# Kernel tuning notes

Hardware: AMD Instinct MI355X
Metric: run time of the kernel (lower is better)

## Reference

```python
import jax, jax.numpy as jnp
import numpy as np

NEG_BIG = -9e15  # matches -9000000000000000.0 in the torch source
ALPHA = 0.2      # LeakyReLU negative slope


def setup_inputs() -> dict:
    key = jax.random.key(0)
    k1, k2, k3, k4 = jax.random.split(key, 4)
    N, F_in, F_out = 8192, 256, 128
    x = jax.random.normal(k1, (N, F_in), dtype=jnp.float32)
    adj = jax.random.randint(k2, (N, N), 0, 2, dtype=jnp.int32)
    W = jax.random.normal(k3, (F_in, F_out), dtype=jnp.float32) * 0.05
    a = jax.random.normal(k4, (2 * F_out, 1), dtype=jnp.float32) * 0.05
    return {"x": x, "adj": adj, "W": W, "a": a}


def reference(x, adj, W, a):
    # h = x @ W : [N, F]
    h = x @ W
    F_out = W.shape[1]
    # Algebraically identical to the concat formulation:
    # a^T [h_i || h_j] = h_i @ a1 + h_j @ a2
    a1 = a[:F_out, 0]
    a2 = a[F_out:, 0]
    src = h @ a1  # [N]
    dst = h @ a2  # [N]
    e = jax.nn.leaky_relu(src[:, None] + dst[None, :], negative_slope=ALPHA)  # [N, N]
    attention = jnp.where(adj > 0, e, NEG_BIG)
    attention = jax.nn.softmax(attention, axis=1)
    # dropout is identity in eval mode (training=False)
    h_prime = attention @ h  # [N, F]
    return h_prime
```

## Files before the change

### kernel.cpp

```cpp
#include <hip/hip_runtime.h>
#include <cstdint>

#define N 8192
#define FIN 256
#define FOUT 128
#define ALPHA 0.2f
#define JP 4
#define JSL (N / JP)
#define TJ 64
#define NTILE (JSL / TJ)
#define RB 32

typedef unsigned short u16;
typedef __attribute__((ext_vector_type(8))) short short8;
typedef __attribute__((ext_vector_type(4))) float floatx4;

__device__ __forceinline__ u16 bf16_rne(float f) {
  uint32_t u = __float_as_uint(f);
  u += 0x7fff + ((u >> 16) & 1);
  return (u16)(u >> 16);
}

__device__ __forceinline__ void gl_lds16(const void* g, void* l) {
  __builtin_amdgcn_global_load_lds(
      (const __attribute__((address_space(1))) void*)g,
      (__attribute__((address_space(3))) void*)l, 16, 0, 0);
}

__global__ __launch_bounds__(256) void k_proj(const float* __restrict__ x,
                                              const float* __restrict__ W,
                                              const float* __restrict__ a,
                                              u16* __restrict__ hT3,
                                              float* __restrict__ srcv,
                                              float* __restrict__ dstv) {
  __shared__ float xs[8 * FIN];
  __shared__ float partS[4][4], partD[4][4];
  const int t = threadIdx.x;
  const int R0 = blockIdx.x * 8;

  const float4* xv = (const float4*)(x + (size_t)R0 * FIN);
  float4* xsv = (float4*)xs;
  xsv[t] = xv[t];
  xsv[t + 256] = xv[t + 256];
  __syncthreads();

  const int c  = t & 127;
  const int rg = (t >> 7) * 4;

  float acc[4] = {0.f, 0.f, 0.f, 0.f};
  float wa[4], wb[4];
  #pragma unroll
  for (int j = 0; j < 4; ++j) wa[j] = W[j * FOUT + c];
  #pragma unroll
  for (int j = 0; j < 4; ++j) wb[j] = W[(4 + j) * FOUT + c];

  for (int k4 = 0; k4 < FIN / 4; ++k4) {
    float wc[4];
    #pragma unroll
    for (int j = 0; j < 4; ++j) { wc[j] = wa[j]; wa[j] = wb[j]; }
    const int kn = (k4 + 2 < FIN / 4) ? k4 + 2 : k4;
    #pragma unroll
    for (int j = 0; j < 4; ++j) wb[j] = W[(kn * 4 + j) * FOUT + c];
    #pragma unroll
    for (int i = 0; i < 4; ++i) {
      const float4 xq = *(const float4*)&xs[(rg + i) * FIN + k4 * 4];
      acc[i] += xq.x * wc[0] + xq.y * wc[1] + xq.z * wc[2] + xq.w * wc[3];
    }
  }

  {
    const int j = R0 + rg;
    const int jb = j >> 5, q = (j >> 3) & 3, jj = j & 7;
    const int m = c & 15, nt = c >> 4;
    union { u16 u[4]; uint2 v; } pk;
    #pragma unroll
    for (int i = 0; i < 4; ++i) pk.u[i] = bf16_rne(acc[i]);
    *(uint2*)(hT3 + (size_t)(((jb * 8 + nt) * 64) + (m * 4 + q)) * 8 + jj) = pk.v;
  }

  const float a1 = a[c], a2 = a[FOUT + c];
  float s4[4], d4[4];
  #pragma unroll
  for (int i = 0; i < 4; ++i) { s4[i] = acc[i] * a1; d4[i] = acc[i] * a2; }
  #pragma unroll
  for (int off = 32; off > 0; off >>= 1) {
    #pragma unroll
    for (int i = 0; i < 4; ++i) {
      s4[i] += __shfl_down(s4[i], off);
      d4[i] += __shfl_down(d4[i], off);
    }
  }
  const int wv = t >> 6, lane = t & 63;
  if (lane == 0) {
    #pragma unroll
    for (int i = 0; i < 4; ++i) { partS[wv][i] = s4[i]; partD[wv][i] = d4[i]; }
  }
  __syncthreads();
  if (t < 16) {
    const int i = t & 3, rg2 = (t >> 2) & 1, which = t >> 3;
    if (which == 0) srcv[R0 + rg2 * 4 + i] = partS[rg2*2][i] + partS[rg2*2+1][i];
    else            dstv[R0 + rg2 * 4 + i] = partD[rg2*2][i] + partD[rg2*2+1][i];
  }
}

__global__ __launch_bounds__(256, 4) void k_gat(const int* __restrict__ adj,
                                                const u16* __restrict__ hT3,
                                                const float* __restrict__ srcv,
                                                const float* __restrict__ dstv,
                                                float* __restrict__ P,
                                                float* __restrict__ lp) {
  __shared__ u16 hS[2][8192];
  const int t = threadIdx.x;
  const int wv = t >> 6, lane = t & 63;
  const int q = lane >> 4, m = lane & 15;
  const int rg = wv & 1;
  const int cg = wv >> 1;
  const int bm = blockIdx.x & 255;
  const int jp = blockIdx.x >> 8;
  const int R0 = bm * RB;
  const int j0 = jp * JSL;
  const int Lq = m * 4 + q;

  const float srcm = srcv[R0 + rg * 16 + m];
  const int*   adjp = adj + (size_t)(R0 + rg * 16 + m) * N + j0 + q * 8;
  const float* dstp = dstv + j0 + q * 8;
  const size_t jb00 = (size_t)(j0 >> 5);

  floatx4 acc[4];
  #pragma unroll
  for (int nt = 0; nt < 4; ++nt) acc[nt] = (floatx4){0.f, 0.f, 0.f, 0.f};
  float lsum = 0.f;

  #define STAGE(I, BUF)                                                        \
  {                                                                            \
    _Pragma("unroll")                                                          \
    for (int cc = 0; cc < 4; ++cc) {                                           \
      const int kc = wv * 4 + cc;                                              \
      const int jbl = kc >> 3, nt_ = kc & 7;                                   \
      const u16* srcp = hT3 + ((jb00 + (size_t)(I) * 2 + jbl) * 8 + nt_) * 512 \
                        + (size_t)lane * 8;                                    \
      gl_lds16(srcp, &hS[BUF][kc * 512]);                                      \
    }                                                                          \
  }

  #define TILE_BODY(I, BUFR, BUFW,                                             \
                    CA0, CA1, CA2, CA3, CD0, CD1, CD2, CD3,                    \
                    NA0, NA1, NA2, NA3, ND0, ND1, ND2, ND3)                    \
  {                                                                            \
    __syncthreads();        \
    const int nx = ((I) + 1 < NTILE) ? (I) + 1 : (I);                          \
    NA0 = *(const int4*)(adjp + nx * TJ);                                      \
    NA1 = *(const int4*)(adjp + nx * TJ + 4);                                  \
    NA2 = *(const int4*)(adjp + nx * TJ + 32);                                 \
    NA3 = *(const int4*)(adjp + nx * TJ + 36);                                 \
    ND0 = *(const float4*)(dstp + nx * TJ);                                    \
    ND1 = *(const float4*)(dstp + nx * TJ + 4);                                \
    ND2 = *(const float4*)(dstp + nx * TJ + 32);                               \
    ND3 = *(const float4*)(dstp + nx * TJ + 36);                               \
    STAGE(nx, BUFW)                                                            \
    _Pragma("unroll")                                                          \
    for (int ks = 0; ks < 2; ++ks) {                                           \
      const int4   A0 = ks ? CA2 : CA0, A1 = ks ? CA3 : CA1;                   \
      const float4 D0 = ks ? CD2 : CD0, D1 = ks ? CD3 : CD1;                   \
      const int   ai[8] = {A0.x, A0.y, A0.z, A0.w, A1.x, A1.y, A1.z, A1.w};    \
      const float df[8] = {D0.x, D0.y, D0.z, D0.w, D1.x, D1.y, D1.z, D1.w};    \
      union { u16 u[8]; short8 s; } pk;                                        \
      _Pragma("unroll")                                                        \
      for (int e = 0; e < 8; ++e) {                                            \
        float v = srcm + df[e];                                                \
        v = fmaxf(v, ALPHA * v);                                               \
        const float p = ai[e] > 0 ? __expf(v) : 0.f;                           \
        lsum += p;                                                             \
        pk.u[e] = bf16_rne(p);                                                 \
      }                                                                        \
      _Pragma("unroll")                                                        \
      for (int nt = 0; nt < 4; ++nt) {                                         \
        const short8 bf =                                                      \
            *(const short8*)&hS[BUFR][(ks * 8 + cg * 4 + nt) * 512 + Lq * 8];  \
        acc[nt] =                                                              \
            __builtin_amdgcn_mfma_f32_16x16x32_bf16(pk.s, bf, acc[nt], 0, 0, 0); \
      }                                                                        \
    }                                                                          \
  }

  int4   aA0 = *(const int4*)(adjp),      aA1 = *(const int4*)(adjp + 4);
  int4   aA2 = *(const int4*)(adjp + 32), aA3 = *(const int4*)(adjp + 36);
  float4 dA0 = *(const float4*)(dstp),      dA1 = *(const float4*)(dstp + 4);
  float4 dA2 = *(const float4*)(dstp + 32), dA3 = *(const float4*)(dstp + 36);
  STAGE(0, 0)
  int4   aB0, aB1, aB2, aB3;
  float4 dB0, dB1, dB2, dB3;

  for (int i = 0; i < NTILE; i += 2) {
    TILE_BODY(i,     (i >> 1) & 0 ? 1 : 0, 1,
              aA0, aA1, aA2, aA3, dA0, dA1, dA2, dA3,
              aB0, aB1, aB2, aB3, dB0, dB1, dB2, dB3)
    TILE_BODY(i + 1, 1, 0,
              aB0, aB1, aB2, aB3, dB0, dB1, dB2, dB3,
              aA0, aA1, aA2, aA3, dA0, dA1, dA2, dA3)
  }
  #undef TILE_BODY
  #undef STAGE

  lsum += __shfl_xor(lsum, 16);
  lsum += __shfl_xor(lsum, 32);
  if (cg == 0 && lane < 16)
    lp[(size_t)jp * N + R0 + rg * 16 + lane] = lsum;

  float* Pp = P + ((size_t)jp * N + R0 + rg * 16) * FOUT + cg * 64;
  #pragma unroll
  for (int nt = 0; nt < 4; ++nt)
    #pragma unroll
    for (int ri = 0; ri < 4; ++ri)
      Pp[(size_t)(q * 4 + ri) * FOUT + nt * 16 + m] = acc[nt][ri];
}

__global__ __launch_bounds__(256) void k_norm(const float* __restrict__ P,
                                              const float* __restrict__ lp,
                                              float* __restrict__ out) {
  const int idx = blockIdx.x * 256 + threadIdx.x;
  const int rr = idx >> 5;
  const int c4 = (idx & 31) * 4;
  float l = 0.f;
  #pragma unroll
  for (int j = 0; j < JP; ++j) l += lp[j * N + rr];
  const float inv = 1.0f / l;
  float4 s = {0.f, 0.f, 0.f, 0.f};
  #pragma unroll
  for (int j = 0; j < JP; ++j) {
    const float4 p = *(const float4*)(P + ((size_t)j * N + rr) * FOUT + c4);
    s.x += p.x; s.y += p.y; s.z += p.z; s.w += p.w;
  }
  s.x *= inv; s.y *= inv; s.z *= inv; s.w *= inv;
  *(float4*)(out + (size_t)rr * FOUT + c4) = s;
}

extern "C" void kernel_launch(void* const* d_in, const int* in_sizes, int n_in,
                              void* d_out, int out_size, void* d_ws, size_t ws_size,
                              hipStream_t stream) {
  const float* x   = (const float*)d_in[0];
  const int*   adj = (const int*)d_in[1];
  const float* W   = (const float*)d_in[2];
  const float* a   = (const float*)d_in[3];
  float* out = (float*)d_out;

  char* ws = (char*)d_ws;
  u16*   hT3  = (u16*)ws;     ws += (size_t)FOUT * N * sizeof(u16);
  float* srcv = (float*)ws;   ws += (size_t)N * sizeof(float);
  float* dstv = (float*)ws;   ws += (size_t)N * sizeof(float);
  float* P    = (float*)ws;   ws += (size_t)JP * N * FOUT * sizeof(float);
  float* lp   = (float*)ws;   ws += (size_t)JP * N * sizeof(float);

  k_proj<<<N / 8, 256, 0, stream>>>(x, W, a, hT3, srcv, dstv);
  k_gat <<<256 * JP, 256, 0, stream>>>(adj, hT3, srcv, dstv, P, lp);
  k_norm<<<(N * FOUT / 4) / 256, 256, 0, stream>>>(P, lp, out);
}
```

Baseline: 456.7 us.

## Pack adjacency into bitmask in a separate pass before attention kernel

Adds a k_mask kernel that reads the int32 adjacency matrix once and packs it into a per-row bitmask using wave ballots. The attention kernel then reads 32x less mask data per tile instead of the full int32 adj rows. The adj/dst register double-buffering is replaced by a simpler loop that loads dst and mask words inline. The adj matrix still has to be read once in full, and in exchange the change adds a kernel launch and a mask buffer in workspace.

```diff
diff --git a/kernel.cpp b/kernel.cpp
--- a/kernel.cpp
+++ b/kernel.cpp
@@ -9,9 +9,9 @@
 #define JSL (N / JP)
 #define TJ 64
 #define NTILE (JSL / TJ)
-#define RB 32
 
 typedef unsigned short u16;
+typedef unsigned int u32;
 typedef __attribute__((ext_vector_type(8))) short short8;
 typedef __attribute__((ext_vector_type(4))) float floatx4;
 
@@ -103,26 +103,50 @@
   }
 }
 
-__global__ __launch_bounds__(256, 4) void k_gat(const int* __restrict__ adj,
+__global__ __launch_bounds__(256, 4) void k_mask(const int* __restrict__ adj,
+                                                 u32* __restrict__ mask) {
+  const int t = threadIdx.x, wv = t >> 6, lane = t & 63;
+  const int row = blockIdx.x * 4 + wv;
+  const int* ar = adj + (size_t)row * N;
+  u32* mr = mask + (size_t)row * (N / 32);
+  const int lh = lane >> 1, ll = lane & 1;
+
+  #pragma unroll 1
+  for (int c = 0; c < 4; ++c) {
+    int v[32];
+    #pragma unroll
+    for (int k = 0; k < 32; ++k) v[k] = ar[c * 2048 + k * 64 + lane];
+    u32 w = 0;
+    #pragma unroll
+    for (int k = 0; k < 32; ++k) {
+      const unsigned long long b = __ballot(v[k] > 0);
+      const u32 cand = ll ? (u32)(b >> 32) : (u32)b;
+      w = (lh == k) ? cand : w;
+    }
+    mr[c * 64 + lane] = w;
+  }
+}
+
+__global__ __launch_bounds__(256, 4) void k_gat(const u32* __restrict__ mask,
                                                 const u16* __restrict__ hT3,
                                                 const float* __restrict__ srcv,
                                                 const float* __restrict__ dstv,
                                                 float* __restrict__ P,
                                                 float* __restrict__ lp) {
   __shared__ u16 hS[2][8192];
-  const int t = threadIdx.x;
-  const int wv = t >> 6, lane = t & 63;
+  const int t = threadIdx.x, wv = t >> 6, lane = t & 63;
   const int q = lane >> 4, m = lane & 15;
   const int rg = wv & 1;
   const int cg = wv >> 1;
   const int bm = blockIdx.x & 255;
   const int jp = blockIdx.x >> 8;
-  const int R0 = bm * RB;
+  const int R0 = bm * 32;
   const int j0 = jp * JSL;
   const int Lq = m * 4 + q;
-
-  const float srcm = srcv[R0 + rg * 16 + m];
-  const int*   adjp = adj + (size_t)(R0 + rg * 16 + m) * N + j0 + q * 8;
+  const int row = R0 + rg * 16 + m;
+
+  const float srcm = srcv[row];
+  const u32*   mrow = mask + (size_t)row * (N / 32) + (j0 >> 5);
   const float* dstp = dstv + j0 + q * 8;
   const size_t jb00 = (size_t)(j0 >> 5);
 
@@ -143,64 +167,48 @@
     }                                                                          \
   }
 
-  #define TILE_BODY(I, BUFR, BUFW,                                             \
-                    CA0, CA1, CA2, CA3, CD0, CD1, CD2, CD3,                    \
-                    NA0, NA1, NA2, NA3, ND0, ND1, ND2, ND3)                    \
+  #define TILE_WORK(I, BUF)                                                    \
   {                                                                            \
-    __syncthreads();        \
-    const int nx = ((I) + 1 < NTILE) ? (I) + 1 : (I);                          \
-    NA0 = *(const int4*)(adjp + nx * TJ);                                      \
-    NA1 = *(const int4*)(adjp + nx * TJ + 4);                                  \
-    NA2 = *(const int4*)(adjp + nx * TJ + 32);                                 \
-    NA3 = *(const int4*)(adjp + nx * TJ + 36);                                 \
-    ND0 = *(const float4*)(dstp + nx * TJ);                                    \
-    ND1 = *(const float4*)(dstp + nx * TJ + 4);                                \
-    ND2 = *(const float4*)(dstp + nx * TJ + 32);                               \
-    ND3 = *(const float4*)(dstp + nx * TJ + 36);                               \
-    STAGE(nx, BUFW)                                                            \
+    const uint2  mw = *(const uint2*)(mrow + (I) * 2);                         \
+    const float4 D0 = *(const float4*)(dstp + (I) * 64);                       \
+    const float4 D1 = *(const float4*)(dstp + (I) * 64 + 4);                   \
+    const float4 D2 = *(const float4*)(dstp + (I) * 64 + 32);                  \
+    const float4 D3 = *(const float4*)(dstp + (I) * 64 + 36);                  \
     _Pragma("unroll")                                                          \
     for (int ks = 0; ks < 2; ++ks) {                                           \
-      const int4   A0 = ks ? CA2 : CA0, A1 = ks ? CA3 : CA1;                   \
-      const float4 D0 = ks ? CD2 : CD0, D1 = ks ? CD3 : CD1;                   \
-      const int   ai[8] = {A0.x, A0.y, A0.z, A0.w, A1.x, A1.y, A1.z, A1.w};    \
-      const float df[8] = {D0.x, D0.y, D0.z, D0.w, D1.x, D1.y, D1.z, D1.w};    \
+      const u32 byte8 = ((ks ? mw.y : mw.x) >> (q * 8)) & 0xffu;               \
+      const float4 Da = ks ? D2 : D0, Db = ks ? D3 : D1;                       \
+      const float df[8] = {Da.x, Da.y, Da.z, Da.w, Db.x, Db.y, Db.z, Db.w};    \
       union { u16 u[8]; short8 s; } pk;                                        \
       _Pragma("unroll")                                                        \
       for (int e = 0; e < 8; ++e) {                                            \
         float v = srcm + df[e];                                                \
         v = fmaxf(v, ALPHA * v);                                               \
-        const float p = ai[e] > 0 ? __expf(v) : 0.f;                           \
+        const float p = ((byte8 >> e) & 1u) ? __expf(v) : 0.f;                 \
         lsum += p;                                                             \
         pk.u[e] = bf16_rne(p);                                                 \
       }                                                                        \
       _Pragma("unroll")                                                        \
       for (int nt = 0; nt < 4; ++nt) {                                         \
         const short8 bf =                                                      \
-            *(const short8*)&hS[BUFR][(ks * 8 + cg * 4 + nt) * 512 + Lq * 8];  \
+            *(const short8*)&hS[BUF][(ks * 8 + cg * 4 + nt) * 512 + Lq * 8];   \
         acc[nt] =                                                              \
             __builtin_amdgcn_mfma_f32_16x16x32_bf16(pk.s, bf, acc[nt], 0, 0, 0); \
       }                                                                        \
     }                                                                          \
   }
 
-  int4   aA0 = *(const int4*)(adjp),      aA1 = *(const int4*)(adjp + 4);
-  int4   aA2 = *(const int4*)(adjp + 32), aA3 = *(const int4*)(adjp + 36);
-  float4 dA0 = *(const float4*)(dstp),      dA1 = *(const float4*)(dstp + 4);
-  float4 dA2 = *(const float4*)(dstp + 32), dA3 = *(const float4*)(dstp + 36);
   STAGE(0, 0)
-  int4   aB0, aB1, aB2, aB3;
-  float4 dB0, dB1, dB2, dB3;
-
   for (int i = 0; i < NTILE; i += 2) {
-    TILE_BODY(i,     (i >> 1) & 0 ? 1 : 0, 1,
-              aA0, aA1, aA2, aA3, dA0, dA1, dA2, dA3,
-              aB0, aB1, aB2, aB3, dB0, dB1, dB2, dB3)
-    TILE_BODY(i + 1, 1, 0,
-              aB0, aB1, aB2, aB3, dB0, dB1, dB2, dB3,
-              aA0, aA1, aA2, aA3, dA0, dA1, dA2, dA3)
-  }
-  #undef TILE_BODY
+    __syncthreads();
+    if (i + 1 < NTILE) STAGE(i + 1, 1)
+    TILE_WORK(i, 0)
+    __syncthreads();
+    if (i + 2 < NTILE) STAGE(i + 2, 0)
+    TILE_WORK(i + 1, 1)
+  }
   #undef STAGE
+  #undef TILE_WORK
 
   lsum += __shfl_xor(lsum, 16);
   lsum += __shfl_xor(lsum, 32);
@@ -223,7 +231,7 @@
   const int c4 = (idx & 31) * 4;
   float l = 0.f;
   #pragma unroll
-  for (int j = 0; j < JP; ++j) l += lp[j * N + rr];
+  for (int j = 0; j < JP; ++j) l += lp[(size_t)j * N + rr];
   const float inv = 1.0f / l;
   float4 s = {0.f, 0.f, 0.f, 0.f};
   #pragma unroll
@@ -248,10 +256,12 @@
   u16*   hT3  = (u16*)ws;     ws += (size_t)FOUT * N * sizeof(u16);
   float* srcv = (float*)ws;   ws += (size_t)N * sizeof(float);
   float* dstv = (float*)ws;   ws += (size_t)N * sizeof(float);
+  u32*   mask = (u32*)ws;     ws += (size_t)N * (N / 32) * sizeof(u32);
   float* P    = (float*)ws;   ws += (size_t)JP * N * FOUT * sizeof(float);
   float* lp   = (float*)ws;   ws += (size_t)JP * N * sizeof(float);
 
   k_proj<<<N / 8, 256, 0, stream>>>(x, W, a, hT3, srcv, dstv);
-  k_gat <<<256 * JP, 256, 0, stream>>>(adj, hT3, srcv, dstv, P, lp);
+  k_mask<<<N / 4, 256, 0, stream>>>(adj, mask);
+  k_gat <<<256 * JP, 256, 0, stream>>>(mask, hT3, srcv, dstv, P, lp);
   k_norm<<<(N * FOUT / 4) / 256, 256, 0, stream>>>(P, lp, out);
 }
```

Measured after the change: 462.4 us. No clear change (+1.2%).
